# Kernel tuning notes

Hardware: AMD Instinct MI355X
Metric: run time of the kernel (lower is better)

Reference implementation:

```python
import jax, jax.numpy as jnp
import numpy as np

WS = (7, 7)          # window size
NUM_HEADS = 4
DIM = 128
B_ = 4096            # batch * num_windows
NW = 256             # num windows per image (mask leading dim)
N = WS[0] * WS[1]    # 49 tokens per window


def _relative_position_index(ws):
    coords = np.stack(np.meshgrid(np.arange(ws[0]), np.arange(ws[1]), indexing='ij'))
    coords = coords.reshape(2, -1)                      # [2, N]
    rel = coords[:, :, None] - coords[:, None, :]       # [2, N, N]
    rel = rel.transpose(1, 2, 0).astype(np.int64)       # [N, N, 2]
    rel[:, :, 0] += ws[0] - 1
    rel[:, :, 1] += ws[1] - 1
    rel[:, :, 0] *= 2 * ws[1] - 1
    return rel.sum(-1)                                  # [N, N] in [0, (2w-1)^2)

REL_POS_INDEX = jnp.asarray(_relative_position_index(WS))


def setup_inputs() -> dict:
    key = jax.random.key(0)
    ks = jax.random.split(key, 4)
    x = jax.random.normal(ks[0], (B_, N, DIM), dtype=jnp.float32)
    mask = jnp.zeros((NW, N, N), dtype=jnp.float32)
    qkv_w = jax.random.normal(ks[1], (DIM, 3 * DIM), dtype=jnp.float32) * 0.02
    qkv_b = jnp.zeros((3 * DIM,), dtype=jnp.float32)
    proj_w = jax.random.normal(ks[2], (DIM, DIM), dtype=jnp.float32) * 0.02
    proj_b = jnp.zeros((DIM,), dtype=jnp.float32)
    bias_table = jax.random.normal(ks[3], ((2 * WS[0] - 1) * (2 * WS[1] - 1), NUM_HEADS), dtype=jnp.float32) * 0.02
    return {"x": x, "mask": mask, "qkv_w": qkv_w, "qkv_b": qkv_b,
            "proj_w": proj_w, "proj_b": proj_b, "bias_table": bias_table}


def reference(x, mask, qkv_w, qkv_b, proj_w, proj_b, bias_table):
    B, n, C = x.shape
    H = NUM_HEADS
    hd = C // H
    scale = hd ** (-0.5)

    qkv = x @ qkv_w + qkv_b                            # [B, N, 3C]
    qkv = qkv.reshape(B, n, 3, H, hd).transpose(2, 0, 3, 1, 4)  # [3, B, H, N, hd]
    q, k, v = qkv[0], qkv[1], qkv[2]

    attn = jnp.einsum('bhnd,bhmd->bhnm', q * scale, k)  # [B, H, N, N]

    # gathered relative-position bias: [N*N, H] -> [H, N, N]
    bias = bias_table[REL_POS_INDEX.reshape(-1)].reshape(n, n, H).transpose(2, 0, 1)
    attn = attn + bias[None]

    nW = mask.shape[0]
    attn = attn.reshape(-1, nW, H, n, n) + mask[None, :, None].astype(attn.dtype)
    attn = attn.reshape(-1, H, n, n)
    attn = jax.nn.softmax(attn, axis=-1)

    out = jnp.einsum('bhnm,bhmd->bnhd', attn, v).reshape(B, n, C)
    out = out @ proj_w + proj_b
    return out
```

## Files before the change

### kernel.cpp

```cpp
#include <hip/hip_runtime.h>
#include <hip/hip_bf16.h>


typedef __attribute__((ext_vector_type(8))) short bf16x8;
typedef __attribute__((ext_vector_type(4))) float f32x4;

#define NTOK  49
#define CDIM  128
#define NWIN  256
#define LDQ   136
#define LDV   72
#define SCALE 0.17677669529663687f
#define PROJ_WOFF 49152

static __device__ __forceinline__ unsigned pk2(float a, float b) {
    __hip_bfloat162 h = __float22bfloat162_rn(make_float2(a, b));
    unsigned u; __builtin_memcpy(&u, &h, 4); return u;
}
static __device__ __forceinline__ short bf1(float a) {
    __hip_bfloat16 h = __float2bfloat16(a);
    unsigned short u; __builtin_memcpy(&u, &h, 2); return (short)u;
}
static __device__ __forceinline__ bf16x8 repack(unsigned p00, unsigned p01,
                                                unsigned p10, unsigned p11,
                                                int src0, int src1, bool hi) {
    union { bf16x8 v; unsigned u[4]; } t;
    unsigned a0, a1;
    a0 = __shfl((int)p00, src0, 64); a1 = __shfl((int)p10, src0, 64); t.u[0] = hi ? a1 : a0;
    a0 = __shfl((int)p01, src0, 64); a1 = __shfl((int)p11, src0, 64); t.u[1] = hi ? a1 : a0;
    a0 = __shfl((int)p00, src1, 64); a1 = __shfl((int)p10, src1, 64); t.u[2] = hi ? a1 : a0;
    a0 = __shfl((int)p01, src1, 64); a1 = __shfl((int)p11, src1, 64); t.u[3] = hi ? a1 : a0;
    return t.v;
}

__global__ void prep_w(const float* __restrict__ qkv_w,
                       const float* __restrict__ proj_w,
                       short* __restrict__ wb) {
    const int fid = blockIdx.x;
    const int l   = threadIdx.x;
    const int lq = l & 15, lg = l >> 4;
    bf16x8 v;
    if (fid < 96) {
        const int nt = fid >> 2, kk = fid & 3;
        #pragma unroll
        for (int j = 0; j < 8; ++j)
            v[j] = bf1(qkv_w[(kk*32 + lg*8 + j)*384 + nt*16 + lq]);
        *(bf16x8*)(wb + fid*512 + l*8) = v;
    } else {
        const int f2 = fid - 96;
        const int nt = f2 >> 2, kk = f2 & 3;
        #pragma unroll
        for (int j = 0; j < 8; ++j)
            v[j] = bf1(proj_w[(kk*32 + lg*8 + j)*128 + nt*16 + lq]);
        *(bf16x8*)(wb + PROJ_WOFF + f2*512 + l*8) = v;
    }
}

__global__ __launch_bounds__(256, 4)
void win_attn(const float* __restrict__ x,
              const float* __restrict__ mask,
              const float* __restrict__ qkv_b,
              const float* __restrict__ proj_b,
              const float* __restrict__ bias_table,
              const short* __restrict__ wb,
              float* __restrict__ out) {
    __shared__ __align__(16) short kl[64 * LDQ];
    __shared__ __align__(16) short vt[128 * LDV];

    const int b    = blockIdx.x;
    const int tid  = threadIdx.x;
    const int l    = tid & 63;
    const int wave = tid >> 6;
    const int lq   = l & 15, lg = l >> 4;
    const int m0   = wave * 16;

    const float* xb = x + (size_t)b * (NTOK * CDIM);
    bf16x8 xf[4][4];
    #pragma unroll
    for (int mt = 0; mt < 4; ++mt) {
        int row = mt*16 + lq; if (row > 48) row = 48;
        const float* pr = xb + row*CDIM + lg*8;
        #pragma unroll
        for (int kk = 0; kk < 4; ++kk) {
            float4 f0 = *(const float4*)(pr + kk*32);
            float4 f1 = *(const float4*)(pr + kk*32 + 4);
            union { bf16x8 v; unsigned u[4]; } t;
            t.u[0] = pk2(f0.x, f0.y);
            t.u[1] = pk2(f0.z, f0.w);
            t.u[2] = pk2(f1.x, f1.y);
            t.u[3] = pk2(f1.z, f1.w);
            xf[mt][kk] = t.v;
        }
    }

    #pragma unroll
    for (int t = 0; t < 4; ++t) {
        const int nt = 8 + wave*4 + t;
        bf16x8 wf[4];
        #pragma unroll
        for (int kk = 0; kk < 4; ++kk)
            wf[kk] = *(const bf16x8*)(wb + (nt*4 + kk)*512 + l*8);
        const f32x4 bia = *(const f32x4*)(qkv_b + nt*16 + lg*4);
        f32x4 acc[4];
        #pragma unroll
        for (int mt = 0; mt < 4; ++mt) acc[mt] = bia;
        #pragma unroll
        for (int kk = 0; kk < 4; ++kk)
            #pragma unroll
            for (int mt = 0; mt < 4; ++mt)
                acc[mt] = __builtin_amdgcn_mfma_f32_16x16x32_bf16(wf[kk], xf[mt][kk], acc[mt], 0, 0, 0);
        if (nt < 16) {
            #pragma unroll
            for (int mt = 0; mt < 4; ++mt) {
                unsigned w0 = pk2(acc[mt][0], acc[mt][1]);
                unsigned w1 = pk2(acc[mt][2], acc[mt][3]);
                *(unsigned long long*)(kl + (mt*16 + lq)*LDQ + (nt - 8)*16 + lg*4) =
                    (unsigned long long)w0 | ((unsigned long long)w1 << 32);
            }
        } else {
            #pragma unroll
            for (int mt = 0; mt < 4; ++mt)
                #pragma unroll
                for (int r = 0; r < 4; ++r)
                    vt[((nt - 16)*16 + lg*4 + r)*LDV + mt*16 + lq] = bf1(acc[mt][r]);
        }
    }

    bf16x8 xa[4];
    #pragma unroll
    for (int mt = 0; mt < 4; ++mt)
        if (wave == mt) {
            #pragma unroll
            for (int kk = 0; kk < 4; ++kk) xa[kk] = xf[mt][kk];
        }
    unsigned qpk[8][2];
    #pragma unroll
    for (int nt = 0; nt < 8; ++nt) {
        bf16x8 wf[4];
        #pragma unroll
        for (int kk = 0; kk < 4; ++kk)
            wf[kk] = *(const bf16x8*)(wb + (nt*4 + kk)*512 + l*8);
        f32x4 acc = *(const f32x4*)(qkv_b + nt*16 + lg*4);
        #pragma unroll
        for (int kk = 0; kk < 4; ++kk)
            acc = __builtin_amdgcn_mfma_f32_16x16x32_bf16(wf[kk], xa[kk], acc, 0, 0, 0);
        qpk[nt][0] = pk2(acc[0]*SCALE, acc[1]*SCALE);
        qpk[nt][1] = pk2(acc[2]*SCALE, acc[3]*SCALE);
    }

    const int qtok = m0 + lq;
    const float* mwin = mask + (size_t)(b & (NWIN - 1)) * (NTOK * NTOK);
    unsigned bmpk[4][4][2];
    {
        const unsigned NEG = pk2(-1e30f, -1e30f);
        #pragma unroll
        for (int nt = 0; nt < 4; ++nt)
            #pragma unroll
            for (int r = 0; r < 4; ++r) {
                const int kt = nt*16 + lg*4 + r;
                if (qtok < NTOK && kt < NTOK) {
                    const int ridx = (qtok/7 - kt/7 + 6)*13 + (qtok%7 - kt%7 + 6);
                    const f32x4 b4 = *(const f32x4*)(bias_table + ridx*4);
                    const float mv = mwin[qtok*NTOK + kt];
                    bmpk[nt][r][0] = pk2(b4[0] + mv, b4[1] + mv);
                    bmpk[nt][r][1] = pk2(b4[2] + mv, b4[3] + mv);
                } else {
                    bmpk[nt][r][0] = NEG; bmpk[nt][r][1] = NEG;
                }
            }
    }
    __syncthreads();

    const int src0 = lq + 16*((2*lg + 0) & 3);
    const int src1 = lq + 16*((2*lg + 1) & 3);
    const bool hi  = (lg >> 1);
    unsigned aopk[8][2];

    #pragma unroll
    for (int h = 0; h < 4; ++h) {
        const bf16x8 qf = repack(qpk[2*h][0], qpk[2*h][1], qpk[2*h+1][0], qpk[2*h+1][1],
                                 src0, src1, hi);
        f32x4 s[4];
        #pragma unroll
        for (int nt = 0; nt < 4; ++nt) {
            bf16x8 kf = *(const bf16x8*)(kl + (nt*16 + lq)*LDQ + h*32 + lg*8);
            f32x4 z = {0.f, 0.f, 0.f, 0.f};
            s[nt] = __builtin_amdgcn_mfma_f32_16x16x32_bf16(kf, qf, z, 0, 0, 0);
        }
        #pragma unroll
        for (int nt = 0; nt < 4; ++nt)
            #pragma unroll
            for (int r = 0; r < 4; ++r) {
                const unsigned u = bmpk[nt][r][h >> 1];
                const float bm = __uint_as_float((h & 1) ? (u & 0xffff0000u) : (u << 16));
                s[nt][r] += bm;
            }
        float mx;
        {
            float m_[4];
            #pragma unroll
            for (int nt = 0; nt < 4; ++nt)
                m_[nt] = fmaxf(fmaxf(s[nt][0], s[nt][1]), fmaxf(s[nt][2], s[nt][3]));
            mx = fmaxf(fmaxf(m_[0], m_[1]), fmaxf(m_[2], m_[3]));
        }
        mx = fmaxf(mx, __shfl_xor(mx, 16, 64));
        mx = fmaxf(mx, __shfl_xor(mx, 32, 64));
        float sum;
        {
            float s_[4];
            #pragma unroll
            for (int nt = 0; nt < 4; ++nt) {
                #pragma unroll
                for (int r = 0; r < 4; ++r)
                    s[nt][r] = __expf(s[nt][r] - mx);
                s_[nt] = (s[nt][0] + s[nt][1]) + (s[nt][2] + s[nt][3]);
            }
            sum = (s_[0] + s_[1]) + (s_[2] + s_[3]);
        }
        sum += __shfl_xor(sum, 16, 64);
        sum += __shfl_xor(sum, 32, 64);
        const float inv = 1.0f / sum;
        unsigned pkv[4][2];
        #pragma unroll
        for (int nt = 0; nt < 4; ++nt) {
            pkv[nt][0] = pk2(s[nt][0]*inv, s[nt][1]*inv);
            pkv[nt][1] = pk2(s[nt][2]*inv, s[nt][3]*inv);
        }
        bf16x8 pa[2];
        #pragma unroll
        for (int c = 0; c < 2; ++c)
            pa[c] = repack(pkv[2*c][0], pkv[2*c][1], pkv[2*c+1][0], pkv[2*c+1][1],
                           src0, src1, hi);
        #pragma unroll
        for (int dn = 0; dn < 2; ++dn) {
            f32x4 o = {0.f, 0.f, 0.f, 0.f};
            #pragma unroll
            for (int kk = 0; kk < 2; ++kk) {
                bf16x8 vf = *(const bf16x8*)(vt + (h*32 + dn*16 + lq)*LDV + kk*32 + lg*8);
                o = __builtin_amdgcn_mfma_f32_16x16x32_bf16(vf, pa[kk], o, 0, 0, 0);
            }
            aopk[2*h + dn][0] = pk2(o[0], o[1]);
            aopk[2*h + dn][1] = pk2(o[2], o[3]);
        }
    }

    bf16x8 ab[4];
    #pragma unroll
    for (int kk = 0; kk < 4; ++kk)
        ab[kk] = repack(aopk[2*kk][0], aopk[2*kk][1], aopk[2*kk+1][0], aopk[2*kk+1][1],
                        src0, src1, hi);
    float* ob = out + (size_t)b * (NTOK * CDIM);
    #pragma unroll
    for (int nt = 0; nt < 8; ++nt) {
        bf16x8 wf[4];
        #pragma unroll
        for (int kk = 0; kk < 4; ++kk)
            wf[kk] = *(const bf16x8*)(wb + PROJ_WOFF + (nt*4 + kk)*512 + l*8);
        const float pb = proj_b[nt*16 + lq];
        f32x4 acc = {pb, pb, pb, pb};
        #pragma unroll
        for (int kk = 0; kk < 4; ++kk)
            acc = __builtin_amdgcn_mfma_f32_16x16x32_bf16(ab[kk], wf[kk], acc, 0, 0, 0);
        #pragma unroll
        for (int r = 0; r < 4; ++r) {
            const int row = m0 + lg*4 + r;
            if (row < NTOK)
                ob[row*CDIM + nt*16 + lq] = acc[r];
        }
    }
}

extern "C" void kernel_launch(void* const* d_in, const int* in_sizes, int n_in,
                              void* d_out, int out_size, void* d_ws, size_t ws_size,
                              hipStream_t stream) {
    (void)in_sizes; (void)n_in; (void)out_size; (void)ws_size;
    const float* x          = (const float*)d_in[0];
    const float* mask       = (const float*)d_in[1];
    const float* qkv_w      = (const float*)d_in[2];
    const float* qkv_b      = (const float*)d_in[3];
    const float* proj_w     = (const float*)d_in[4];
    const float* proj_b     = (const float*)d_in[5];
    const float* bias_table = (const float*)d_in[6];
    float* out = (float*)d_out;
    short* wb  = (short*)d_ws;

    hipLaunchKernelGGL(prep_w,   dim3(128),  dim3(64),  0, stream, qkv_w, proj_w, wb);
    hipLaunchKernelGGL(win_attn, dim3(4096), dim3(256), 0, stream,
                       x, mask, qkv_b, proj_b, bias_table, wb, out);
}
```

Before: 138.5 us.

## Compute K/V per-wave for own tokens, XOR-swizzle LDS, vectorize output stores

```diff
diff --git a/kernel.cpp b/kernel.cpp
--- a/kernel.cpp
+++ b/kernel.cpp
@@ -8,8 +8,6 @@
 #define NTOK  49
 #define CDIM  128
 #define NWIN  256
-#define LDQ   136
-#define LDV   72
 #define SCALE 0.17677669529663687f
 #define PROJ_WOFF 49152
 
@@ -56,7 +54,7 @@
     }
 }
 
-__global__ __launch_bounds__(256, 4)
+__global__ __launch_bounds__(256, 5)
 void win_attn(const float* __restrict__ x,
               const float* __restrict__ mask,
               const float* __restrict__ qkv_b,
@@ -64,8 +62,8 @@
               const float* __restrict__ bias_table,
               const short* __restrict__ wb,
               float* __restrict__ out) {
-    __shared__ __align__(16) short kl[64 * LDQ];
-    __shared__ __align__(16) short vt[128 * LDV];
+    __shared__ __align__(16) short kl[64 * 128];
+    __shared__ __align__(16) short vt[128 * 64];
 
     const int b    = blockIdx.x;
     const int tid  = threadIdx.x;
@@ -73,12 +71,12 @@
     const int wave = tid >> 6;
     const int lq   = l & 15, lg = l >> 4;
     const int m0   = wave * 16;
+    const int qtok = m0 + lq;
 
     const float* xb = x + (size_t)b * (NTOK * CDIM);
-    bf16x8 xf[4][4];
-    #pragma unroll
-    for (int mt = 0; mt < 4; ++mt) {
-        int row = mt*16 + lq; if (row > 48) row = 48;
+    bf16x8 xa[4];
+    {
+        int row = qtok; if (row > 48) row = 48;
         const float* pr = xb + row*CDIM + lg*8;
         #pragma unroll
         for (int kk = 0; kk < 4; ++kk) {
@@ -89,53 +87,13 @@
             t.u[1] = pk2(f0.z, f0.w);
             t.u[2] = pk2(f1.x, f1.y);
             t.u[3] = pk2(f1.z, f1.w);
-            xf[mt][kk] = t.v;
-        }
-    }
-
-    #pragma unroll
-    for (int t = 0; t < 4; ++t) {
-        const int nt = 8 + wave*4 + t;
-        bf16x8 wf[4];
-        #pragma unroll
-        for (int kk = 0; kk < 4; ++kk)
-            wf[kk] = *(const bf16x8*)(wb + (nt*4 + kk)*512 + l*8);
-        const f32x4 bia = *(const f32x4*)(qkv_b + nt*16 + lg*4);
-        f32x4 acc[4];
-        #pragma unroll
-        for (int mt = 0; mt < 4; ++mt) acc[mt] = bia;
-        #pragma unroll
-        for (int kk = 0; kk < 4; ++kk)
-            #pragma unroll
-            for (int mt = 0; mt < 4; ++mt)
-                acc[mt] = __builtin_amdgcn_mfma_f32_16x16x32_bf16(wf[kk], xf[mt][kk], acc[mt], 0, 0, 0);
-        if (nt < 16) {
-            #pragma unroll
-            for (int mt = 0; mt < 4; ++mt) {
-                unsigned w0 = pk2(acc[mt][0], acc[mt][1]);
-                unsigned w1 = pk2(acc[mt][2], acc[mt][3]);
-                *(unsigned long long*)(kl + (mt*16 + lq)*LDQ + (nt - 8)*16 + lg*4) =
-                    (unsigned long long)w0 | ((unsigned long long)w1 << 32);
-            }
-        } else {
-            #pragma unroll
-            for (int mt = 0; mt < 4; ++mt)
-                #pragma unroll
-                for (int r = 0; r < 4; ++r)
-                    vt[((nt - 16)*16 + lg*4 + r)*LDV + mt*16 + lq] = bf1(acc[mt][r]);
-        }
-    }
-
-    bf16x8 xa[4];
-    #pragma unroll
-    for (int mt = 0; mt < 4; ++mt)
-        if (wave == mt) {
-            #pragma unroll
-            for (int kk = 0; kk < 4; ++kk) xa[kk] = xf[mt][kk];
-        }
+            xa[kk] = t.v;
+        }
+    }
+
     unsigned qpk[8][2];
     #pragma unroll
-    for (int nt = 0; nt < 8; ++nt) {
+    for (int nt = 0; nt < 24; ++nt) {
         bf16x8 wf[4];
         #pragma unroll
         for (int kk = 0; kk < 4; ++kk)
@@ -144,11 +102,25 @@
         #pragma unroll
         for (int kk = 0; kk < 4; ++kk)
             acc = __builtin_amdgcn_mfma_f32_16x16x32_bf16(wf[kk], xa[kk], acc, 0, 0, 0);
-        qpk[nt][0] = pk2(acc[0]*SCALE, acc[1]*SCALE);
-        qpk[nt][1] = pk2(acc[2]*SCALE, acc[3]*SCALE);
-    }
-
-    const int qtok = m0 + lq;
+        if (nt < 8) {
+            qpk[nt][0] = pk2(acc[0]*SCALE, acc[1]*SCALE);
+            qpk[nt][1] = pk2(acc[2]*SCALE, acc[3]*SCALE);
+        } else if (nt < 16) {
+            unsigned w0 = pk2(acc[0], acc[1]);
+            unsigned w1 = pk2(acc[2], acc[3]);
+            const int ub  = (nt - 8)*2 + (lg >> 1);
+            const int off = qtok*128 + ((ub ^ (qtok & 7)) << 3) + (lg & 1)*4;
+            *(unsigned long long*)(kl + off) =
+                (unsigned long long)w0 | ((unsigned long long)w1 << 32);
+        } else {
+            #pragma unroll
+            for (int r = 0; r < 4; ++r) {
+                const int dim = (nt - 16)*16 + lg*4 + r;
+                vt[dim*64 + (((qtok >> 3) ^ (dim & 7)) << 3) + (qtok & 7)] = bf1(acc[r]);
+            }
+        }
+    }
+
     const float* mwin = mask + (size_t)(b & (NWIN - 1)) * (NTOK * NTOK);
     unsigned bmpk[4][4][2];
     {
@@ -183,7 +155,9 @@
         f32x4 s[4];
         #pragma unroll
         for (int nt = 0; nt < 4; ++nt) {
-            bf16x8 kf = *(const bf16x8*)(kl + (nt*16 + lq)*LDQ + h*32 + lg*8);
+            const int krow = nt*16 + lq;
+            const int u    = h*4 + lg;
+            bf16x8 kf = *(const bf16x8*)(kl + krow*128 + ((u ^ (krow & 7)) << 3));
             f32x4 z = {0.f, 0.f, 0.f, 0.f};
             s[nt] = __builtin_amdgcn_mfma_f32_16x16x32_bf16(kf, qf, z, 0, 0, 0);
         }
@@ -236,7 +210,9 @@
             f32x4 o = {0.f, 0.f, 0.f, 0.f};
             #pragma unroll
             for (int kk = 0; kk < 2; ++kk) {
-                bf16x8 vf = *(const bf16x8*)(vt + (h*32 + dn*16 + lq)*LDV + kk*32 + lg*8);
+                const int dim = h*32 + dn*16 + lq;
+                const int u   = kk*4 + lg;
+                bf16x8 vf = *(const bf16x8*)(vt + dim*64 + ((u ^ (dim & 7)) << 3));
                 o = __builtin_amdgcn_mfma_f32_16x16x32_bf16(vf, pa[kk], o, 0, 0, 0);
             }
             aopk[2*h + dn][0] = pk2(o[0], o[1]);
@@ -256,17 +232,12 @@
         #pragma unroll
         for (int kk = 0; kk < 4; ++kk)
             wf[kk] = *(const bf16x8*)(wb + PROJ_WOFF + (nt*4 + kk)*512 + l*8);
-        const float pb = proj_b[nt*16 + lq];
-        f32x4 acc = {pb, pb, pb, pb};
-        #pragma unroll
-        for (int kk = 0; kk < 4; ++kk)
-            acc = __builtin_amdgcn_mfma_f32_16x16x32_bf16(ab[kk], wf[kk], acc, 0, 0, 0);
-        #pragma unroll
-        for (int r = 0; r < 4; ++r) {
-            const int row = m0 + lg*4 + r;
-            if (row < NTOK)
-                ob[row*CDIM + nt*16 + lq] = acc[r];
-        }
+        f32x4 acc = *(const f32x4*)(proj_b + nt*16 + lg*4);
+        #pragma unroll
+        for (int kk = 0; kk < 4; ++kk)
+            acc = __builtin_amdgcn_mfma_f32_16x16x32_bf16(wf[kk], ab[kk], acc, 0, 0, 0);
+        if (qtok < NTOK)
+            *(f32x4*)(ob + qtok*CDIM + nt*16 + lg*4) = acc;
     }
 }
 
```

New measurement: 132.8 us. -4.1%, faster.

## Split window attention by head per wave, keep QKV in registers

Applied to the files above, without the earlier changes.

```diff
diff --git a/kernel.cpp b/kernel.cpp
--- a/kernel.cpp
+++ b/kernel.cpp
@@ -8,8 +8,7 @@
 #define NTOK  49
 #define CDIM  128
 #define NWIN  256
-#define LDQ   136
-#define LDV   72
+#define LDA   136
 #define SCALE 0.17677669529663687f
 #define PROJ_WOFF 49152
 
@@ -56,7 +55,7 @@
     }
 }
 
-__global__ __launch_bounds__(256, 4)
+__global__ __launch_bounds__(256, 2)
 void win_attn(const float* __restrict__ x,
               const float* __restrict__ mask,
               const float* __restrict__ qkv_b,
@@ -64,18 +63,16 @@
               const float* __restrict__ bias_table,
               const short* __restrict__ wb,
               float* __restrict__ out) {
-    __shared__ __align__(16) short kl[64 * LDQ];
-    __shared__ __align__(16) short vt[128 * LDV];
-
-    const int b    = blockIdx.x;
-    const int tid  = threadIdx.x;
-    const int l    = tid & 63;
-    const int wave = tid >> 6;
-    const int lq   = l & 15, lg = l >> 4;
-    const int m0   = wave * 16;
+    __shared__ __align__(16) short ao_lds[64 * LDA];
+
+    const int b   = blockIdx.x;
+    const int tid = threadIdx.x;
+    const int l   = tid & 63;
+    const int wv  = tid >> 6;
+    const int lq  = l & 15, lg = l >> 4;
 
     const float* xb = x + (size_t)b * (NTOK * CDIM);
-    bf16x8 xf[4][4];
+    bf16x8 xa[4][4];
     #pragma unroll
     for (int mt = 0; mt < 4; ++mt) {
         int row = mt*16 + lq; if (row > 48) row = 48;
@@ -89,118 +86,140 @@
             t.u[1] = pk2(f0.z, f0.w);
             t.u[2] = pk2(f1.x, f1.y);
             t.u[3] = pk2(f1.z, f1.w);
-            xf[mt][kk] = t.v;
-        }
-    }
-
-    #pragma unroll
-    for (int t = 0; t < 4; ++t) {
-        const int nt = 8 + wave*4 + t;
-        bf16x8 wf[4];
-        #pragma unroll
-        for (int kk = 0; kk < 4; ++kk)
-            wf[kk] = *(const bf16x8*)(wb + (nt*4 + kk)*512 + l*8);
-        const f32x4 bia = *(const f32x4*)(qkv_b + nt*16 + lg*4);
-        f32x4 acc[4];
-        #pragma unroll
-        for (int mt = 0; mt < 4; ++mt) acc[mt] = bia;
-        #pragma unroll
-        for (int kk = 0; kk < 4; ++kk)
-            #pragma unroll
-            for (int mt = 0; mt < 4; ++mt)
-                acc[mt] = __builtin_amdgcn_mfma_f32_16x16x32_bf16(wf[kk], xf[mt][kk], acc[mt], 0, 0, 0);
-        if (nt < 16) {
+            xa[mt][kk] = t.v;
+        }
+    }
+
+    unsigned qpk[2][4][2], kpk[2][4][2], vpk[2][4][2];
+    #pragma unroll
+    for (int t = 0; t < 2; ++t) {
+        {
+            const int nt = 2*wv + t;
+            bf16x8 wf[4];
+            #pragma unroll
+            for (int kk = 0; kk < 4; ++kk)
+                wf[kk] = *(const bf16x8*)(wb + (nt*4 + kk)*512 + l*8);
+            const f32x4 bia = *(const f32x4*)(qkv_b + nt*16 + lg*4);
+            f32x4 acc[4];
+            #pragma unroll
+            for (int mt = 0; mt < 4; ++mt) acc[mt] = bia;
+            #pragma unroll
+            for (int kk = 0; kk < 4; ++kk)
+                #pragma unroll
+                for (int mt = 0; mt < 4; ++mt)
+                    acc[mt] = __builtin_amdgcn_mfma_f32_16x16x32_bf16(wf[kk], xa[mt][kk], acc[mt], 0, 0, 0);
             #pragma unroll
             for (int mt = 0; mt < 4; ++mt) {
-                unsigned w0 = pk2(acc[mt][0], acc[mt][1]);
-                unsigned w1 = pk2(acc[mt][2], acc[mt][3]);
-                *(unsigned long long*)(kl + (mt*16 + lq)*LDQ + (nt - 8)*16 + lg*4) =
-                    (unsigned long long)w0 | ((unsigned long long)w1 << 32);
-            }
-        } else {
-            #pragma unroll
-            for (int mt = 0; mt < 4; ++mt)
+                qpk[t][mt][0] = pk2(acc[mt][0]*SCALE, acc[mt][1]*SCALE);
+                qpk[t][mt][1] = pk2(acc[mt][2]*SCALE, acc[mt][3]*SCALE);
+            }
+        }
+        {
+            const int nt = 8 + 2*wv + t;
+            bf16x8 wf[4];
+            #pragma unroll
+            for (int kk = 0; kk < 4; ++kk)
+                wf[kk] = *(const bf16x8*)(wb + (nt*4 + kk)*512 + l*8);
+            const f32x4 bia = *(const f32x4*)(qkv_b + nt*16 + lg*4);
+            f32x4 acc[4];
+            #pragma unroll
+            for (int mt = 0; mt < 4; ++mt) acc[mt] = bia;
+            #pragma unroll
+            for (int kk = 0; kk < 4; ++kk)
                 #pragma unroll
-                for (int r = 0; r < 4; ++r)
-                    vt[((nt - 16)*16 + lg*4 + r)*LDV + mt*16 + lq] = bf1(acc[mt][r]);
-        }
-    }
-
-    bf16x8 xa[4];
-    #pragma unroll
-    for (int mt = 0; mt < 4; ++mt)
-        if (wave == mt) {
-            #pragma unroll
-            for (int kk = 0; kk < 4; ++kk) xa[kk] = xf[mt][kk];
-        }
-    unsigned qpk[8][2];
-    #pragma unroll
-    for (int nt = 0; nt < 8; ++nt) {
-        bf16x8 wf[4];
-        #pragma unroll
-        for (int kk = 0; kk < 4; ++kk)
-            wf[kk] = *(const bf16x8*)(wb + (nt*4 + kk)*512 + l*8);
-        f32x4 acc = *(const f32x4*)(qkv_b + nt*16 + lg*4);
-        #pragma unroll
-        for (int kk = 0; kk < 4; ++kk)
-            acc = __builtin_amdgcn_mfma_f32_16x16x32_bf16(wf[kk], xa[kk], acc, 0, 0, 0);
-        qpk[nt][0] = pk2(acc[0]*SCALE, acc[1]*SCALE);
-        qpk[nt][1] = pk2(acc[2]*SCALE, acc[3]*SCALE);
-    }
-
-    const int qtok = m0 + lq;
+                for (int mt = 0; mt < 4; ++mt)
+                    acc[mt] = __builtin_amdgcn_mfma_f32_16x16x32_bf16(wf[kk], xa[mt][kk], acc[mt], 0, 0, 0);
+            #pragma unroll
+            for (int mt = 0; mt < 4; ++mt) {
+                kpk[t][mt][0] = pk2(acc[mt][0], acc[mt][1]);
+                kpk[t][mt][1] = pk2(acc[mt][2], acc[mt][3]);
+            }
+        }
+        {
+            const int nt = 16 + 2*wv + t;
+            bf16x8 wf[4];
+            #pragma unroll
+            for (int kk = 0; kk < 4; ++kk)
+                wf[kk] = *(const bf16x8*)(wb + (nt*4 + kk)*512 + l*8);
+            const float bv = qkv_b[nt*16 + lq];
+            f32x4 acc[4];
+            #pragma unroll
+            for (int mt = 0; mt < 4; ++mt) acc[mt] = (f32x4){bv, bv, bv, bv};
+            #pragma unroll
+            for (int kk = 0; kk < 4; ++kk)
+                #pragma unroll
+                for (int mt = 0; mt < 4; ++mt)
+                    acc[mt] = __builtin_amdgcn_mfma_f32_16x16x32_bf16(xa[mt][kk], wf[kk], acc[mt], 0, 0, 0);
+            #pragma unroll
+            for (int mt = 0; mt < 4; ++mt) {
+                vpk[t][mt][0] = pk2(acc[mt][0], acc[mt][1]);
+                vpk[t][mt][1] = pk2(acc[mt][2], acc[mt][3]);
+            }
+        }
+    }
+
     const float* mwin = mask + (size_t)(b & (NWIN - 1)) * (NTOK * NTOK);
     unsigned bmpk[4][4][2];
-    {
-        const unsigned NEG = pk2(-1e30f, -1e30f);
-        #pragma unroll
-        for (int nt = 0; nt < 4; ++nt)
+    #pragma unroll
+    for (int mtq = 0; mtq < 4; ++mtq) {
+        const int qtok = mtq*16 + lq;
+        #pragma unroll
+        for (int mtk = 0; mtk < 4; ++mtk) {
+            float bm[4];
             #pragma unroll
             for (int r = 0; r < 4; ++r) {
-                const int kt = nt*16 + lg*4 + r;
+                const int kt = mtk*16 + lg*4 + r;
+                bm[r] = -1e30f;
                 if (qtok < NTOK && kt < NTOK) {
                     const int ridx = (qtok/7 - kt/7 + 6)*13 + (qtok%7 - kt%7 + 6);
-                    const f32x4 b4 = *(const f32x4*)(bias_table + ridx*4);
-                    const float mv = mwin[qtok*NTOK + kt];
-                    bmpk[nt][r][0] = pk2(b4[0] + mv, b4[1] + mv);
-                    bmpk[nt][r][1] = pk2(b4[2] + mv, b4[3] + mv);
-                } else {
-                    bmpk[nt][r][0] = NEG; bmpk[nt][r][1] = NEG;
+                    bm[r] = bias_table[ridx*4 + wv] + mwin[qtok*NTOK + kt];
                 }
             }
-    }
-    __syncthreads();
+            bmpk[mtq][mtk][0] = pk2(bm[0], bm[1]);
+            bmpk[mtq][mtk][1] = pk2(bm[2], bm[3]);
+        }
+    }
 
     const int src0 = lq + 16*((2*lg + 0) & 3);
     const int src1 = lq + 16*((2*lg + 1) & 3);
     const bool hi  = (lg >> 1);
-    unsigned aopk[8][2];
-
-    #pragma unroll
-    for (int h = 0; h < 4; ++h) {
-        const bf16x8 qf = repack(qpk[2*h][0], qpk[2*h][1], qpk[2*h+1][0], qpk[2*h+1][1],
+
+    bf16x8 kf[4];
+    #pragma unroll
+    for (int mtk = 0; mtk < 4; ++mtk)
+        kf[mtk] = repack(kpk[0][mtk][0], kpk[0][mtk][1], kpk[1][mtk][0], kpk[1][mtk][1],
+                         src0, src1, hi);
+    bf16x8 vf[2][2];
+    #pragma unroll
+    for (int dv = 0; dv < 2; ++dv)
+        #pragma unroll
+        for (int c = 0; c < 2; ++c)
+            vf[dv][c] = repack(vpk[dv][2*c][0], vpk[dv][2*c][1],
+                               vpk[dv][2*c+1][0], vpk[dv][2*c+1][1], src0, src1, hi);
+
+    #pragma unroll
+    for (int mtq = 0; mtq < 4; ++mtq) {
+        const bf16x8 qf = repack(qpk[0][mtq][0], qpk[0][mtq][1], qpk[1][mtq][0], qpk[1][mtq][1],
                                  src0, src1, hi);
         f32x4 s[4];
         #pragma unroll
-        for (int nt = 0; nt < 4; ++nt) {
-            bf16x8 kf = *(const bf16x8*)(kl + (nt*16 + lq)*LDQ + h*32 + lg*8);
+        for (int mtk = 0; mtk < 4; ++mtk) {
             f32x4 z = {0.f, 0.f, 0.f, 0.f};
-            s[nt] = __builtin_amdgcn_mfma_f32_16x16x32_bf16(kf, qf, z, 0, 0, 0);
-        }
-        #pragma unroll
-        for (int nt = 0; nt < 4; ++nt)
+            s[mtk] = __builtin_amdgcn_mfma_f32_16x16x32_bf16(kf[mtk], qf, z, 0, 0, 0);
+        }
+        #pragma unroll
+        for (int mtk = 0; mtk < 4; ++mtk)
             #pragma unroll
             for (int r = 0; r < 4; ++r) {
-                const unsigned u = bmpk[nt][r][h >> 1];
-                const float bm = __uint_as_float((h & 1) ? (u & 0xffff0000u) : (u << 16));
-                s[nt][r] += bm;
+                const unsigned u = bmpk[mtq][mtk][r >> 1];
+                s[mtk][r] += __uint_as_float((r & 1) ? (u & 0xffff0000u) : (u << 16));
             }
         float mx;
         {
             float m_[4];
             #pragma unroll
-            for (int nt = 0; nt < 4; ++nt)
-                m_[nt] = fmaxf(fmaxf(s[nt][0], s[nt][1]), fmaxf(s[nt][2], s[nt][3]));
+            for (int mtk = 0; mtk < 4; ++mtk)
+                m_[mtk] = fmaxf(fmaxf(s[mtk][0], s[mtk][1]), fmaxf(s[mtk][2], s[mtk][3]));
             mx = fmaxf(fmaxf(m_[0], m_[1]), fmaxf(m_[2], m_[3]));
         }
         mx = fmaxf(mx, __shfl_xor(mx, 16, 64));
@@ -209,11 +228,11 @@
         {
             float s_[4];
             #pragma unroll
-            for (int nt = 0; nt < 4; ++nt) {
+            for (int mtk = 0; mtk < 4; ++mtk) {
                 #pragma unroll
                 for (int r = 0; r < 4; ++r)
-                    s[nt][r] = __expf(s[nt][r] - mx);
-                s_[nt] = (s[nt][0] + s[nt][1]) + (s[nt][2] + s[nt][3]);
+                    s[mtk][r] = __expf(s[mtk][r] - mx);
+                s_[mtk] = (s[mtk][0] + s[mtk][1]) + (s[mtk][2] + s[mtk][3]);
             }
             sum = (s_[0] + s_[1]) + (s_[2] + s_[3]);
         }
@@ -222,9 +241,9 @@
         const float inv = 1.0f / sum;
         unsigned pkv[4][2];
         #pragma unroll
-        for (int nt = 0; nt < 4; ++nt) {
-            pkv[nt][0] = pk2(s[nt][0]*inv, s[nt][1]*inv);
-            pkv[nt][1] = pk2(s[nt][2]*inv, s[nt][3]*inv);
+        for (int mtk = 0; mtk < 4; ++mtk) {
+            pkv[mtk][0] = pk2(s[mtk][0]*inv, s[mtk][1]*inv);
+            pkv[mtk][1] = pk2(s[mtk][2]*inv, s[mtk][3]*inv);
         }
         bf16x8 pa[2];
         #pragma unroll
@@ -232,40 +251,38 @@
             pa[c] = repack(pkv[2*c][0], pkv[2*c][1], pkv[2*c+1][0], pkv[2*c+1][1],
                            src0, src1, hi);
         #pragma unroll
-        for (int dn = 0; dn < 2; ++dn) {
+        for (int dv = 0; dv < 2; ++dv) {
             f32x4 o = {0.f, 0.f, 0.f, 0.f};
-            #pragma unroll
-            for (int kk = 0; kk < 2; ++kk) {
-                bf16x8 vf = *(const bf16x8*)(vt + (h*32 + dn*16 + lq)*LDV + kk*32 + lg*8);
-                o = __builtin_amdgcn_mfma_f32_16x16x32_bf16(vf, pa[kk], o, 0, 0, 0);
-            }
-            aopk[2*h + dn][0] = pk2(o[0], o[1]);
-            aopk[2*h + dn][1] = pk2(o[2], o[3]);
-        }
-    }
-
-    bf16x8 ab[4];
-    #pragma unroll
-    for (int kk = 0; kk < 4; ++kk)
-        ab[kk] = repack(aopk[2*kk][0], aopk[2*kk][1], aopk[2*kk+1][0], aopk[2*kk+1][1],
-                        src0, src1, hi);
+            o = __builtin_amdgcn_mfma_f32_16x16x32_bf16(vf[dv][0], pa[0], o, 0, 0, 0);
+            o = __builtin_amdgcn_mfma_f32_16x16x32_bf16(vf[dv][1], pa[1], o, 0, 0, 0);
+            unsigned w0 = pk2(o[0], o[1]);
+            unsigned w1 = pk2(o[2], o[3]);
+            *(unsigned long long*)(ao_lds + (mtq*16 + lq)*LDA + wv*32 + dv*16 + lg*4) =
+                (unsigned long long)w0 | ((unsigned long long)w1 << 32);
+        }
+    }
+    __syncthreads();
+
     float* ob = out + (size_t)b * (NTOK * CDIM);
     #pragma unroll
-    for (int nt = 0; nt < 8; ++nt) {
+    for (int t = 0; t < 2; ++t) {
+        const int nto = 2*wv + t;
         bf16x8 wf[4];
         #pragma unroll
         for (int kk = 0; kk < 4; ++kk)
-            wf[kk] = *(const bf16x8*)(wb + PROJ_WOFF + (nt*4 + kk)*512 + l*8);
-        const float pb = proj_b[nt*16 + lq];
-        f32x4 acc = {pb, pb, pb, pb};
-        #pragma unroll
-        for (int kk = 0; kk < 4; ++kk)
-            acc = __builtin_amdgcn_mfma_f32_16x16x32_bf16(ab[kk], wf[kk], acc, 0, 0, 0);
-        #pragma unroll
-        for (int r = 0; r < 4; ++r) {
-            const int row = m0 + lg*4 + r;
-            if (row < NTOK)
-                ob[row*CDIM + nt*16 + lq] = acc[r];
+            wf[kk] = *(const bf16x8*)(wb + PROJ_WOFF + (nto*4 + kk)*512 + l*8);
+        const f32x4 pbv = *(const f32x4*)(proj_b + nto*16 + lg*4);
+        #pragma unroll
+        for (int mt = 0; mt < 4; ++mt) {
+            f32x4 acc = pbv;
+            #pragma unroll
+            for (int kk = 0; kk < 4; ++kk) {
+                bf16x8 ab = *(const bf16x8*)(ao_lds + (mt*16 + lq)*LDA + kk*32 + lg*8);
+                acc = __builtin_amdgcn_mfma_f32_16x16x32_bf16(wf[kk], ab, acc, 0, 0, 0);
+            }
+            const int tok = mt*16 + lq;
+            if (tok < NTOK)
+                *(f32x4*)(ob + tok*CDIM + nto*16 + lg*4) = acc;
         }
     }
 }
```

Measured after the change: 171.9 us. 24.1% more time.
